# Kernel optimization log

Hardware: AMD Instinct MI355X
Metric: run time of the kernel (lower is better)

## Reference

```python
import jax, jax.numpy as jnp
import numpy as np

B, H, W, F, D = 8, 126, 126, 64, 32
ITERS, NIT = 3, 20
RHO, NU, DT, FRC = 1.0, 0.1, 0.1, 1.0
DX = 2.0 / (B + 1)
DY = 2.0 / (H + 1)
DX2, DY2 = DX * DX, DY * DY
DEN = 2.0 * (DX2 + DY2)


def _b_term(du_dx, dv_dy, du_dy, dv_dx):
    return RHO * ((du_dx + dv_dy) / DT - du_dx**2 - 2.0 * du_dy * dv_dx - dv_dy**2)


def build_b(u, v):
    b = jnp.zeros_like(u)
    # interior
    b = b.at[:, 1:-1, 1:-1].set(_b_term(
        (u[:, 1:-1, 2:] - u[:, 1:-1, :-2]) / (2 * DX),
        (v[:, 2:, 1:-1] - v[:, :-2, 1:-1]) / (2 * DY),
        (u[:, 2:, 1:-1] - u[:, :-2, 1:-1]) / (2 * DY),
        (v[:, 1:-1, 2:] - v[:, 1:-1, :-2]) / (2 * DX)))
    # periodic wrap, last column
    b = b.at[:, 1:-1, -1].set(_b_term(
        (u[:, 1:-1, 0] - u[:, 1:-1, -2]) / (2 * DX),
        (v[:, 2:, -1] - v[:, :-2, -1]) / (2 * DY),
        (u[:, 2:, -1] - u[:, :-2, -1]) / (2 * DY),
        (v[:, 1:-1, 0] - v[:, 1:-1, -2]) / (2 * DX)))
    # periodic wrap, first column
    b = b.at[:, 1:-1, 0].set(_b_term(
        (u[:, 1:-1, 1] - u[:, 1:-1, -1]) / (2 * DX),
        (v[:, 2:, 0] - v[:, :-2, 0]) / (2 * DY),
        (u[:, 2:, 0] - u[:, :-2, 0]) / (2 * DY),
        (v[:, 1:-1, 1] - v[:, 1:-1, -1]) / (2 * DX)))
    return b


def pressure_poisson(p, b):
    c = DX2 * DY2 / DEN

    def step(p, _):
        pn = p
        p = p.at[:, 1:-1, 1:-1].set(
            ((pn[:, 1:-1, 2:] + pn[:, 1:-1, :-2]) * DY2 + (pn[:, 2:, 1:-1] + pn[:, :-2, 1:-1]) * DX2) / DEN
            - c * b[:, 1:-1, 1:-1])
        p = p.at[:, 1:-1, -1].set(
            ((pn[:, 1:-1, 0] + pn[:, 1:-1, -2]) * DY2 + (pn[:, 2:, -1] + pn[:, :-2, -1]) * DX2) / DEN
            - c * b[:, 1:-1, -1])
        p = p.at[:, 1:-1, 0].set(
            ((pn[:, 1:-1, 1] + pn[:, 1:-1, -1]) * DY2 + (pn[:, 2:, 0] + pn[:, :-2, 0]) * DX2) / DEN
            - c * b[:, 1:-1, 0])
        # Neumann-style row boundaries (copy from updated p, as in torch code)
        p = p.at[:, -1].set(p[:, -2])
        p = p.at[:, 0].set(p[:, 1])
        return p, None

    p, _ = jax.lax.scan(step, p, None, length=NIT)
    return p


def velocity_step(u, v, p):
    un, vn = u, v
    uc = un[:, 1:-1, 1:-1]
    vc = vn[:, 1:-1, 1:-1]
    u_i = (uc - uc * DT / DX * (uc - un[:, 1:-1, :-2]) - vc * DT / DY * (uc - un[:, :-2, 1:-1])
           - DT / (2 * RHO * DX) * (p[:, 1:-1, 2:] - p[:, 1:-1, :-2])
           + NU * (DT / DX2 * (un[:, 1:-1, 2:] - 2 * uc + un[:, 1:-1, :-2])
                   + DT / DY2 * (un[:, 2:, 1:-1] - 2 * uc + un[:, :-2, 1:-1]))
           + FRC * DT)
    v_i = (vc - uc * DT / DX * (vc - vn[:, 1:-1, :-2]) - vc * DT / DY * (vc - vn[:, :-2, 1:-1])
           - DT / (2 * RHO * DY) * (p[:, 2:, 1:-1] - p[:, :-2, 1:-1])
           + NU * (DT / DX2 * (vn[:, 1:-1, 2:] - 2 * vc + vn[:, 1:-1, :-2])
                   + DT / DY2 * (vn[:, 2:, 1:-1] - 2 * vc + vn[:, :-2, 1:-1])))
    ue = un[:, 1:-1, -1]
    ve = vn[:, 1:-1, -1]
    u_e = (ue - ue * DT / DX * (ue - un[:, 1:-1, -2]) - ve * DT / DY * (ue - un[:, :-2, -1])
           - DT / (2 * RHO * DX) * (p[:, 1:-1, 0] - p[:, 1:-1, -2])
           + NU * (DT / DX2 * (un[:, 1:-1, 0] - 2 * ue + un[:, 1:-1, -2])
                   + DT / DY2 * (un[:, 2:, -1] - 2 * ue + un[:, :-2, -1]))
           + FRC * DT)
    v_e = (ve - ue * DT / DX * (ve - vn[:, 1:-1, -2]) - ve * DT / DY * (ve - vn[:, :-2, -1])
           - DT / (2 * RHO * DY) * (p[:, 2:, -1] - p[:, :-2, -1])
           + NU * (DT / DX2 * (vn[:, 1:-1, 0] - 2 * ve + vn[:, 1:-1, -2])
                   + DT / DY2 * (vn[:, 2:, -1] - 2 * ve + vn[:, :-2, -1])))
    u0c = un[:, 1:-1, 0]
    v0c = vn[:, 1:-1, 0]
    u_0 = (u0c - u0c * DT / DX * (u0c - un[:, 1:-1, -1]) - v0c * DT / DY * (u0c - un[:, :-2, 0])
           - DT / (2 * RHO * DX) * (p[:, 1:-1, 1] - p[:, 1:-1, -1])
           + NU * (DT / DX2 * (un[:, 1:-1, 1] - 2 * u0c + un[:, 1:-1, -1])
                   + DT / DY2 * (un[:, 2:, 0] - 2 * u0c + un[:, :-2, 0]))
           + FRC * DT)
    v_0 = (v0c - u0c * DT / DX * (v0c - vn[:, 1:-1, -1]) - v0c * DT / DY * (v0c - vn[:, :-2, 0])
           - DT / (2 * RHO * DY) * (p[:, 2:, 0] - p[:, :-2, 0])
           + NU * (DT / DX2 * (vn[:, 1:-1, 1] - 2 * v0c + vn[:, 1:-1, -1])
                   + DT / DY2 * (vn[:, 2:, 0] - 2 * v0c + vn[:, :-2, 0])))
    u = un.at[:, 1:-1, 1:-1].set(u_i).at[:, 1:-1, -1].set(u_e).at[:, 1:-1, 0].set(u_0)
    v = vn.at[:, 1:-1, 1:-1].set(v_i).at[:, 1:-1, -1].set(v_e).at[:, 1:-1, 0].set(v_0)
    u = u.at[:, 0].set(0.0).at[:, -1].set(0.0)
    v = v.at[:, 0].set(0.0).at[:, -1].set(0.0)
    return u, v


def setup_inputs() -> dict:
    key = jax.random.key(0)
    ks = jax.random.split(key, 5)
    x = jax.random.normal(ks[0], (B, H, W, F), jnp.float32) * 0.05
    u0 = jax.random.normal(ks[1], (B, H + 2, W + 2, D), jnp.float32) * 0.05
    v0 = jax.random.normal(ks[2], (B, H + 2, W + 2, D), jnp.float32) * 0.05
    w = jax.random.normal(ks[3], (D, F), jnp.float32) / np.float32(np.sqrt(F))
    b_lin = jax.random.normal(ks[4], (D,), jnp.float32) * 0.01
    return {"x": x, "u0": u0, "v0": v0, "w": w, "b_lin": b_lin}


def reference(x, u0, v0, w, b_lin):
    # pad spatial dims by 1 then linear preprocess: (B,H+2,W+2,F) -> (B,H+2,W+2,D)
    p = jnp.pad(x, ((0, 0), (1, 1), (1, 1), (0, 0)))
    p = jnp.einsum('bhwf,df->bhwd', p, w) + b_lin
    u, v = u0, v0
    for _ in range(ITERS):
        b = build_b(u, v)
        p = pressure_poisson(p, b)
        u, v = velocity_step(u, v, p)
    return p[:, -1, :, :]  # (B, W+2, D)
```

## Files before the change

### kernel.cpp

```cpp
#include <hip/hip_runtime.h>

#define NITER 20
#define OUTER 3

constexpr double DXd  = 2.0 / 9.0;
constexpr double DYd  = 2.0 / 127.0;
constexpr double DX2d = DXd * DXd;
constexpr double DY2d = DYd * DYd;
constexpr double DENd = 2.0 * (DX2d + DY2d);

constexpr float K1     = (float)(DY2d / DENd);
constexpr float K2     = (float)(DX2d / DENd);
constexpr float CC     = (float)(DX2d * DY2d / DENd);
constexpr float INV2DX = (float)(1.0 / (2.0 * DXd));
constexpr float INV2DY = (float)(1.0 / (2.0 * DYd));
constexpr float INVDT  = (float)(1.0 / 0.1);
constexpr float DTDX   = (float)(0.1 / DXd);
constexpr float DTDY   = (float)(0.1 / DYd);
constexpr float PGX    = (float)(0.1 / (2.0 * 1.0 * DXd));
constexpr float PGY    = (float)(0.1 / (2.0 * 1.0 * DYd));
constexpr float A1     = (float)(0.1 / DX2d);
constexpr float A2     = (float)(0.1 / DY2d);
constexpr float NUf    = 0.1f;
constexpr float FDT    = 0.1f;

__device__ __forceinline__ float bperm(int srcByte, float v) {
    return __int_as_float(__builtin_amdgcn_ds_bpermute(srcByte, __float_as_int(v)));
}

__global__ __launch_bounds__(256) void einsum_kernel(
    const float* __restrict__ x, const float* __restrict__ w,
    const float* __restrict__ bl, float* __restrict__ p0)
{
    int id = blockIdx.x * 256 + threadIdx.x;
    int c = id & 127, r = (id >> 7) & 127, b = id >> 14;
    float acc[32];
#pragma unroll
    for (int d = 0; d < 32; ++d) acc[d] = bl[d];
    if (r >= 1 && r <= 126 && c >= 1 && c <= 126) {
        const float* xp = x + (((size_t)(b * 126 + (r - 1))) * 126 + (c - 1)) * 64;
#pragma unroll
        for (int f = 0; f < 64; f += 4) {
            float4 xv = *(const float4*)(xp + f);
#pragma unroll
            for (int d = 0; d < 32; ++d) {
                acc[d] += xv.x * w[d * 64 + f] + xv.y * w[d * 64 + f + 1]
                        + xv.z * w[d * 64 + f + 2] + xv.w * w[d * 64 + f + 3];
            }
        }
    }
    float* op = p0 + ((size_t)b * 32) * 16384 + r * 128 + c;
#pragma unroll
    for (int d = 0; d < 32; ++d) op[(size_t)d * 16384] = acc[d];
}

__global__ __launch_bounds__(512, 2) void sim_kernel(
    const float* __restrict__ u0, const float* __restrict__ v0,
    const float* __restrict__ p0ws, const float* __restrict__ x,
    const float* __restrict__ w, const float* __restrict__ bl,
    float* __restrict__ out, int use_ws)
{
    __shared__ float sP[2][16][2][128];
    __shared__ float sU[16][2][128];
    __shared__ float sV[16][2][128];

    const int tid = threadIdx.x;
    const int tx = tid & 31, ty = tid >> 5;
    const int c0 = tx << 2, r0 = ty << 3;
    const int lane = tid & 63;
    const int srcL = (((lane & 32) | ((lane + 31) & 31)) << 2);
    const int srcR = (((lane & 32) | ((lane + 1) & 31)) << 2);
    const int bb = blockIdx.x & 7;
    const int d  = blockIdx.x >> 3;

    float pC[8][4], uC[8][4], vC[8][4], cb[8][4];

#pragma unroll
    for (int r = 0; r < 8; ++r) {
        const size_t base = ((size_t)((bb * 128 + (r0 + r)) * 128 + c0)) * 32 + d;
#pragma unroll
        for (int c = 0; c < 4; ++c) {
            uC[r][c] = u0[base + (size_t)c * 32];
            vC[r][c] = v0[base + (size_t)c * 32];
        }
    }

    if (use_ws) {
        const float* pp = p0ws + ((size_t)(bb * 32 + d)) * 16384;
#pragma unroll
        for (int r = 0; r < 8; ++r) {
            float4 t = *(const float4*)(pp + (r0 + r) * 128 + c0);
            pC[r][0] = t.x; pC[r][1] = t.y; pC[r][2] = t.z; pC[r][3] = t.w;
        }
    } else {
        const float blv = bl[d];
#pragma unroll
        for (int r = 0; r < 8; ++r) {
            const int gr = r0 + r;
#pragma unroll
            for (int c = 0; c < 4; ++c) {
                const int gc = c0 + c;
                float acc = blv;
                if (gr >= 1 && gr <= 126 && gc >= 1 && gc <= 126) {
                    const float* xp = x + (((size_t)(bb * 126 + (gr - 1))) * 126 + (gc - 1)) * 64;
                    for (int f = 0; f < 64; f += 4) {
                        float4 xv = *(const float4*)(xp + f);
                        acc += xv.x * w[d * 64 + f] + xv.y * w[d * 64 + f + 1]
                             + xv.z * w[d * 64 + f + 2] + xv.w * w[d * 64 + f + 3];
                    }
                }
                pC[r][c] = acc;
            }
        }
    }

    int s = 0;
    *(float4*)&sP[0][ty][0][c0] = make_float4(pC[0][0], pC[0][1], pC[0][2], pC[0][3]);
    *(float4*)&sP[0][ty][1][c0] = make_float4(pC[7][0], pC[7][1], pC[7][2], pC[7][3]);
    *(float4*)&sU[ty][0][c0]    = make_float4(uC[0][0], uC[0][1], uC[0][2], uC[0][3]);
    *(float4*)&sU[ty][1][c0]    = make_float4(uC[7][0], uC[7][1], uC[7][2], uC[7][3]);
    *(float4*)&sV[ty][0][c0]    = make_float4(vC[0][0], vC[0][1], vC[0][2], vC[0][3]);
    *(float4*)&sV[ty][1][c0]    = make_float4(vC[7][0], vC[7][1], vC[7][2], vC[7][3]);
    __syncthreads();

    const int tyN = (ty > 0) ? ty - 1 : 0;
    const int tyS = (ty < 15) ? ty + 1 : 15;

    for (int outer = 0; outer < OUTER; ++outer) {
        {
            float4 uN4 = *(const float4*)&sU[tyN][1][c0];
            float4 uS4 = *(const float4*)&sU[tyS][0][c0];
            float4 vN4 = *(const float4*)&sV[tyN][1][c0];
            float4 vS4 = *(const float4*)&sV[tyS][0][c0];
            float uNh[4] = {uN4.x, uN4.y, uN4.z, uN4.w};
            float uSh[4] = {uS4.x, uS4.y, uS4.z, uS4.w};
            float vNh[4] = {vN4.x, vN4.y, vN4.z, vN4.w};
            float vSh[4] = {vS4.x, vS4.y, vS4.z, vS4.w};
#pragma unroll
            for (int r = 0; r < 8; ++r) {
                const int gr = r0 + r;
                const bool valid = (gr >= 1) && (gr <= 126);
                float uWh = bperm(srcL, uC[r][3]);
                float uEh = bperm(srcR, uC[r][0]);
                float vWh = bperm(srcL, vC[r][3]);
                float vEh = bperm(srcR, vC[r][0]);
#pragma unroll
                for (int c = 0; c < 4; ++c) {
                    float uE = (c < 3) ? uC[r][c + 1] : uEh;
                    float uW = (c > 0) ? uC[r][c - 1] : uWh;
                    float vE = (c < 3) ? vC[r][c + 1] : vEh;
                    float vW = (c > 0) ? vC[r][c - 1] : vWh;
                    float uN = (r > 0) ? uC[r - 1][c] : uNh[c];
                    float uS = (r < 7) ? uC[r + 1][c] : uSh[c];
                    float vN = (r > 0) ? vC[r - 1][c] : vNh[c];
                    float vS = (r < 7) ? vC[r + 1][c] : vSh[c];
                    float dudx = (uE - uW) * INV2DX;
                    float dvdy = (vS - vN) * INV2DY;
                    float dudy = (uS - uN) * INV2DY;
                    float dvdx = (vE - vW) * INV2DX;
                    float bt = (dudx + dvdy) * INVDT - dudx * dudx
                             - 2.0f * dudy * dvdx - dvdy * dvdy;
                    cb[r][c] = valid ? CC * bt : 0.0f;
                }
            }
        }

        for (int it = 0; it < NITER; ++it) {
            float4 t4 = *(const float4*)&sP[s][tyN][1][c0];
            float4 b4 = *(const float4*)&sP[s][tyS][0][c0];
            float nrow[4] = {t4.x, t4.y, t4.z, t4.w};
            float shalo[4] = {b4.x, b4.y, b4.z, b4.w};
#pragma unroll
            for (int r = 0; r < 8; ++r) {
                const int gr = r0 + r;
                const bool valid = (gr >= 1) && (gr <= 126);
                float old0[4];
#pragma unroll
                for (int c = 0; c < 4; ++c) old0[c] = pC[r][c];
                float pWh = bperm(srcL, old0[3]);
                float pEh = bperm(srcR, old0[0]);
#pragma unroll
                for (int c = 0; c < 4; ++c) {
                    float E = (c < 3) ? old0[c + 1] : pEh;
                    float W = (c > 0) ? old0[c - 1] : pWh;
                    float N = nrow[c];
                    float S = (r < 7) ? pC[r + 1][c] : shalo[c];
                    float nv = (E + W) * K1 + (N + S) * K2 - cb[r][c];
                    pC[r][c] = valid ? nv : old0[c];
                }
#pragma unroll
                for (int c = 0; c < 4; ++c) nrow[c] = old0[c];
            }
            if (ty == 0) {
#pragma unroll
                for (int c = 0; c < 4; ++c) pC[0][c] = pC[1][c];
            }
            if (ty == 15) {
#pragma unroll
                for (int c = 0; c < 4; ++c) pC[7][c] = pC[6][c];
            }
            *(float4*)&sP[s ^ 1][ty][0][c0] = make_float4(pC[0][0], pC[0][1], pC[0][2], pC[0][3]);
            *(float4*)&sP[s ^ 1][ty][1][c0] = make_float4(pC[7][0], pC[7][1], pC[7][2], pC[7][3]);
            __syncthreads();
            s ^= 1;
        }

        {
            float4 ut4 = *(const float4*)&sU[tyN][1][c0];
            float4 us4 = *(const float4*)&sU[tyS][0][c0];
            float4 vt4 = *(const float4*)&sV[tyN][1][c0];
            float4 vs4 = *(const float4*)&sV[tyS][0][c0];
            float4 pt4 = *(const float4*)&sP[s][tyN][1][c0];
            float4 pb4 = *(const float4*)&sP[s][tyS][0][c0];
            float uNh[4] = {ut4.x, ut4.y, ut4.z, ut4.w};
            float uSh[4] = {us4.x, us4.y, us4.z, us4.w};
            float vNh[4] = {vt4.x, vt4.y, vt4.z, vt4.w};
            float vSh[4] = {vs4.x, vs4.y, vs4.z, vs4.w};
            float pNh[4] = {pt4.x, pt4.y, pt4.z, pt4.w};
            float pSh[4] = {pb4.x, pb4.y, pb4.z, pb4.w};
            __syncthreads();

            float uNrow[4], vNrow[4];
#pragma unroll
            for (int c = 0; c < 4; ++c) { uNrow[c] = uNh[c]; vNrow[c] = vNh[c]; }
#pragma unroll
            for (int r = 0; r < 8; ++r) {
                const int gr = r0 + r;
                const bool valid = (gr >= 1) && (gr <= 126);
                float uold[4], vold[4];
#pragma unroll
                for (int c = 0; c < 4; ++c) { uold[c] = uC[r][c]; vold[c] = vC[r][c]; }
                float uWh = bperm(srcL, uold[3]);
                float uEh = bperm(srcR, uold[0]);
                float vWh = bperm(srcL, vold[3]);
                float vEh = bperm(srcR, vold[0]);
                float pWh = bperm(srcL, pC[r][3]);
                float pEh = bperm(srcR, pC[r][0]);
#pragma unroll
                for (int c = 0; c < 4; ++c) {
                    float uc = uold[c], vc = vold[c];
                    float uE = (c < 3) ? uold[c + 1] : uEh;
                    float uW = (c > 0) ? uold[c - 1] : uWh;
                    float vE = (c < 3) ? vold[c + 1] : vEh;
                    float vW = (c > 0) ? vold[c - 1] : vWh;
                    float uN = uNrow[c];
                    float uS = (r < 7) ? uC[r + 1][c] : uSh[c];
                    float vN = vNrow[c];
                    float vS = (r < 7) ? vC[r + 1][c] : vSh[c];
                    float pE = (c < 3) ? pC[r][c + 1] : pEh;
                    float pW = (c > 0) ? pC[r][c - 1] : pWh;
                    float pN = (r > 0) ? pC[r - 1][c] : pNh[c];
                    float pS = (r < 7) ? pC[r + 1][c] : pSh[c];

                    float unew = uc - uc * DTDX * (uc - uW) - vc * DTDY * (uc - uN)
                               - PGX * (pE - pW)
                               + NUf * (A1 * (uE - 2.0f * uc + uW) + A2 * (uS - 2.0f * uc + uN))
                               + FDT;
                    float vnew = vc - uc * DTDX * (vc - vW) - vc * DTDY * (vc - vN)
                               - PGY * (pS - pN)
                               + NUf * (A1 * (vE - 2.0f * vc + vW) + A2 * (vS - 2.0f * vc + vN));
                    uC[r][c] = valid ? unew : uc;
                    vC[r][c] = valid ? vnew : vc;
                }
#pragma unroll
                for (int c = 0; c < 4; ++c) { uNrow[c] = uold[c]; vNrow[c] = vold[c]; }
            }
            if (ty == 0) {
#pragma unroll
                for (int c = 0; c < 4; ++c) { uC[0][c] = 0.0f; vC[0][c] = 0.0f; }
            }
            if (ty == 15) {
#pragma unroll
                for (int c = 0; c < 4; ++c) { uC[7][c] = 0.0f; vC[7][c] = 0.0f; }
            }
            *(float4*)&sU[ty][0][c0] = make_float4(uC[0][0], uC[0][1], uC[0][2], uC[0][3]);
            *(float4*)&sU[ty][1][c0] = make_float4(uC[7][0], uC[7][1], uC[7][2], uC[7][3]);
            *(float4*)&sV[ty][0][c0] = make_float4(vC[0][0], vC[0][1], vC[0][2], vC[0][3]);
            *(float4*)&sV[ty][1][c0] = make_float4(vC[7][0], vC[7][1], vC[7][2], vC[7][3]);
            __syncthreads();
        }
    }

    if (ty == 15) {
        float* op = out + ((size_t)bb * 128 + c0) * 32 + d;
        op[0]  = pC[7][0];
        op[32] = pC[7][1];
        op[64] = pC[7][2];
        op[96] = pC[7][3];
    }
}

extern "C" void kernel_launch(void* const* d_in, const int* in_sizes, int n_in,
                              void* d_out, int out_size, void* d_ws, size_t ws_size,
                              hipStream_t stream) {
    const float* x  = (const float*)d_in[0];
    const float* u0 = (const float*)d_in[1];
    const float* v0 = (const float*)d_in[2];
    const float* w  = (const float*)d_in[3];
    const float* bl = (const float*)d_in[4];
    float* out = (float*)d_out;
    float* p0  = (float*)d_ws;

    const size_t need = (size_t)8 * 32 * 128 * 128 * sizeof(float);
    const int use_ws = (ws_size >= need) ? 1 : 0;

    if (use_ws) {
        einsum_kernel<<<512, 256, 0, stream>>>(x, w, bl, p0);
    }
    sim_kernel<<<256, 512, 0, stream>>>(u0, v0, p0, x, w, bl, out, use_ws);
}
```

Baseline: 267.0 us.

## Fuse einsum preprocessing into sim kernel and drop row-validity selects

Removes the separate einsum kernel and its workspace round-trip. Each sim block now computes its own initial pressure channel, using the weight row preloaded into registers as float4. It also drops the per-row valid selects in the b, Poisson and velocity updates, relying on later boundary overwrites for rows 0 and 127. The Poisson loop now hoists all eight lane permutes ahead of the row loop. The risk is that the fused preprocessing reads x with a strided per-thread pattern, repeated across 32 d-blocks per batch, which may be slower than the dedicated kernel.

```diff
diff --git a/kernel.cpp b/kernel.cpp
--- a/kernel.cpp
+++ b/kernel.cpp
@@ -14,11 +14,11 @@
 constexpr float CC     = (float)(DX2d * DY2d / DENd);
 constexpr float INV2DX = (float)(1.0 / (2.0 * DXd));
 constexpr float INV2DY = (float)(1.0 / (2.0 * DYd));
-constexpr float INVDT  = (float)(1.0 / 0.1);
+constexpr float INVDT  = 10.0f;
 constexpr float DTDX   = (float)(0.1 / DXd);
 constexpr float DTDY   = (float)(0.1 / DYd);
-constexpr float PGX    = (float)(0.1 / (2.0 * 1.0 * DXd));
-constexpr float PGY    = (float)(0.1 / (2.0 * 1.0 * DYd));
+constexpr float PGX    = (float)(0.1 / (2.0 * DXd));
+constexpr float PGY    = (float)(0.1 / (2.0 * DYd));
 constexpr float A1     = (float)(0.1 / DX2d);
 constexpr float A2     = (float)(0.1 / DY2d);
 constexpr float NUf    = 0.1f;
@@ -28,37 +28,10 @@
     return __int_as_float(__builtin_amdgcn_ds_bpermute(srcByte, __float_as_int(v)));
 }
 
-__global__ __launch_bounds__(256) void einsum_kernel(
-    const float* __restrict__ x, const float* __restrict__ w,
-    const float* __restrict__ bl, float* __restrict__ p0)
-{
-    int id = blockIdx.x * 256 + threadIdx.x;
-    int c = id & 127, r = (id >> 7) & 127, b = id >> 14;
-    float acc[32];
-#pragma unroll
-    for (int d = 0; d < 32; ++d) acc[d] = bl[d];
-    if (r >= 1 && r <= 126 && c >= 1 && c <= 126) {
-        const float* xp = x + (((size_t)(b * 126 + (r - 1))) * 126 + (c - 1)) * 64;
-#pragma unroll
-        for (int f = 0; f < 64; f += 4) {
-            float4 xv = *(const float4*)(xp + f);
-#pragma unroll
-            for (int d = 0; d < 32; ++d) {
-                acc[d] += xv.x * w[d * 64 + f] + xv.y * w[d * 64 + f + 1]
-                        + xv.z * w[d * 64 + f + 2] + xv.w * w[d * 64 + f + 3];
-            }
-        }
-    }
-    float* op = p0 + ((size_t)b * 32) * 16384 + r * 128 + c;
-#pragma unroll
-    for (int d = 0; d < 32; ++d) op[(size_t)d * 16384] = acc[d];
-}
-
 __global__ __launch_bounds__(512, 2) void sim_kernel(
     const float* __restrict__ u0, const float* __restrict__ v0,
-    const float* __restrict__ p0ws, const float* __restrict__ x,
-    const float* __restrict__ w, const float* __restrict__ bl,
-    float* __restrict__ out, int use_ws)
+    const float* __restrict__ x,  const float* __restrict__ w,
+    const float* __restrict__ bl, float* __restrict__ out)
 {
     __shared__ float sP[2][16][2][128];
     __shared__ float sU[16][2][128];
@@ -75,42 +48,37 @@
 
     float pC[8][4], uC[8][4], vC[8][4], cb[8][4];
 
-#pragma unroll
-    for (int r = 0; r < 8; ++r) {
-        const size_t base = ((size_t)((bb * 128 + (r0 + r)) * 128 + c0)) * 32 + d;
-#pragma unroll
-        for (int c = 0; c < 4; ++c) {
-            uC[r][c] = u0[base + (size_t)c * 32];
-            vC[r][c] = v0[base + (size_t)c * 32];
-        }
-    }
-
-    if (use_ws) {
-        const float* pp = p0ws + ((size_t)(bb * 32 + d)) * 16384;
-#pragma unroll
-        for (int r = 0; r < 8; ++r) {
-            float4 t = *(const float4*)(pp + (r0 + r) * 128 + c0);
-            pC[r][0] = t.x; pC[r][1] = t.y; pC[r][2] = t.z; pC[r][3] = t.w;
-        }
-    } else {
+    {
+        float4 wv[16];
+#pragma unroll
+        for (int i = 0; i < 16; ++i) wv[i] = *(const float4*)(w + d * 64 + i * 4);
         const float blv = bl[d];
-#pragma unroll
         for (int r = 0; r < 8; ++r) {
             const int gr = r0 + r;
-#pragma unroll
             for (int c = 0; c < 4; ++c) {
                 const int gc = c0 + c;
                 float acc = blv;
                 if (gr >= 1 && gr <= 126 && gc >= 1 && gc <= 126) {
                     const float* xp = x + (((size_t)(bb * 126 + (gr - 1))) * 126 + (gc - 1)) * 64;
-                    for (int f = 0; f < 64; f += 4) {
-                        float4 xv = *(const float4*)(xp + f);
-                        acc += xv.x * w[d * 64 + f] + xv.y * w[d * 64 + f + 1]
-                             + xv.z * w[d * 64 + f + 2] + xv.w * w[d * 64 + f + 3];
+#pragma unroll
+                    for (int i = 0; i < 16; ++i) {
+                        float4 xv = *(const float4*)(xp + 4 * i);
+                        acc += xv.x * wv[i].x + xv.y * wv[i].y
+                             + xv.z * wv[i].z + xv.w * wv[i].w;
                     }
                 }
                 pC[r][c] = acc;
             }
+        }
+    }
+
+#pragma unroll
+    for (int r = 0; r < 8; ++r) {
+        const size_t base = ((size_t)((bb * 128 + (r0 + r)) * 128 + c0)) * 32 + d;
+#pragma unroll
+        for (int c = 0; c < 4; ++c) {
+            uC[r][c] = u0[base + (size_t)c * 32];
+            vC[r][c] = v0[base + (size_t)c * 32];
         }
     }
 
@@ -138,8 +106,6 @@
             float vSh[4] = {vS4.x, vS4.y, vS4.z, vS4.w};
 #pragma unroll
             for (int r = 0; r < 8; ++r) {
-                const int gr = r0 + r;
-                const bool valid = (gr >= 1) && (gr <= 126);
                 float uWh = bperm(srcL, uC[r][3]);
                 float uEh = bperm(srcR, uC[r][0]);
                 float vWh = bperm(srcL, vC[r][3]);
@@ -160,7 +126,7 @@
                     float dvdx = (vE - vW) * INV2DX;
                     float bt = (dudx + dvdy) * INVDT - dudx * dudx
                              - 2.0f * dudy * dvdx - dvdy * dvdy;
-                    cb[r][c] = valid ? CC * bt : 0.0f;
+                    cb[r][c] = -(CC * bt);
                 }
             }
         }
@@ -168,25 +134,26 @@
         for (int it = 0; it < NITER; ++it) {
             float4 t4 = *(const float4*)&sP[s][tyN][1][c0];
             float4 b4 = *(const float4*)&sP[s][tyS][0][c0];
+            float pWh[8], pEh[8];
+#pragma unroll
+            for (int r = 0; r < 8; ++r) {
+                pWh[r] = bperm(srcL, pC[r][3]);
+                pEh[r] = bperm(srcR, pC[r][0]);
+            }
             float nrow[4] = {t4.x, t4.y, t4.z, t4.w};
             float shalo[4] = {b4.x, b4.y, b4.z, b4.w};
 #pragma unroll
             for (int r = 0; r < 8; ++r) {
-                const int gr = r0 + r;
-                const bool valid = (gr >= 1) && (gr <= 126);
                 float old0[4];
 #pragma unroll
                 for (int c = 0; c < 4; ++c) old0[c] = pC[r][c];
-                float pWh = bperm(srcL, old0[3]);
-                float pEh = bperm(srcR, old0[0]);
 #pragma unroll
                 for (int c = 0; c < 4; ++c) {
-                    float E = (c < 3) ? old0[c + 1] : pEh;
-                    float W = (c > 0) ? old0[c - 1] : pWh;
+                    float E = (c < 3) ? old0[c + 1] : pEh[r];
+                    float W = (c > 0) ? old0[c - 1] : pWh[r];
                     float N = nrow[c];
                     float S = (r < 7) ? pC[r + 1][c] : shalo[c];
-                    float nv = (E + W) * K1 + (N + S) * K2 - cb[r][c];
-                    pC[r][c] = valid ? nv : old0[c];
+                    pC[r][c] = (E + W) * K1 + ((N + S) * K2 + cb[r][c]);
                 }
 #pragma unroll
                 for (int c = 0; c < 4; ++c) nrow[c] = old0[c];
@@ -225,8 +192,6 @@
             for (int c = 0; c < 4; ++c) { uNrow[c] = uNh[c]; vNrow[c] = vNh[c]; }
 #pragma unroll
             for (int r = 0; r < 8; ++r) {
-                const int gr = r0 + r;
-                const bool valid = (gr >= 1) && (gr <= 126);
                 float uold[4], vold[4];
 #pragma unroll
                 for (int c = 0; c < 4; ++c) { uold[c] = uC[r][c]; vold[c] = vC[r][c]; }
@@ -259,8 +224,8 @@
                     float vnew = vc - uc * DTDX * (vc - vW) - vc * DTDY * (vc - vN)
                                - PGY * (pS - pN)
                                + NUf * (A1 * (vE - 2.0f * vc + vW) + A2 * (vS - 2.0f * vc + vN));
-                    uC[r][c] = valid ? unew : uc;
-                    vC[r][c] = valid ? vnew : vc;
+                    uC[r][c] = unew;
+                    vC[r][c] = vnew;
                 }
 #pragma unroll
                 for (int c = 0; c < 4; ++c) { uNrow[c] = uold[c]; vNrow[c] = vold[c]; }
@@ -299,13 +264,7 @@
     const float* w  = (const float*)d_in[3];
     const float* bl = (const float*)d_in[4];
     float* out = (float*)d_out;
-    float* p0  = (float*)d_ws;
-
-    const size_t need = (size_t)8 * 32 * 128 * 128 * sizeof(float);
-    const int use_ws = (ws_size >= need) ? 1 : 0;
-
-    if (use_ws) {
-        einsum_kernel<<<512, 256, 0, stream>>>(x, w, bl, p0);
-    }
-    sim_kernel<<<256, 512, 0, stream>>>(u0, v0, p0, x, w, bl, out, use_ws);
+    (void)d_ws; (void)ws_size;
+
+    sim_kernel<<<256, 512, 0, stream>>>(u0, v0, x, w, bl, out);
 }
```

After: 297.2 us. 1.11x slower.
